# Optimization experiments

Measured on AMD Instinct MI355X. Metric: run time of the kernel, lower is better.

Reference implementation:

```python
import jax, jax.numpy as jnp
import numpy as np

B, F, T, K = 4096, 2048, 16, 8


def setup_inputs() -> dict:
    key = jax.random.key(0)
    k1, k2, k3 = jax.random.split(key, 3)
    h_ens = jax.random.normal(k1, (B, F, T), dtype=jnp.float32)
    # Stacked per-(task, timestep) Linear(num_in_feat, 1) weights and biases.
    # nn.Linear default init ~ U(-1/sqrt(F), 1/sqrt(F)); plain normals are fine for a numeric reference.
    W = jax.random.normal(k2, (K, T, F), dtype=jnp.float32) * (1.0 / np.sqrt(F))
    b = jax.random.normal(k3, (K, T), dtype=jnp.float32) * (1.0 / np.sqrt(F))
    return {"h_ens": h_ens, "W": W, "b": b}


def reference(h_ens, W, b):
    # h_ens: [B, F, T], W: [K, T, F], b: [K, T]
    # logits[b, t, k] = sum_f h_ens[b, f, t] * W[k, t, f] + b[k, t]
    logits = jnp.einsum('bft,ktf->btk', h_ens, W) + b.T[None, :, :]
    return jax.nn.sigmoid(logits)  # [B, T, K]
```

## Files before the change

kernel.cpp:

```cpp
#include <hip/hip_runtime.h>
#include <math.h>

#define B_TOT 4096
#define F_DIM 2048
#define T_DIM 16
#define K_DIM 8
#define NB    4
#define SF    64
#define NSUP  (F_DIM / SF)

__device__ __forceinline__ void gload_lds16(const float* g, float* l) {
    __builtin_amdgcn_global_load_lds(
        (const __attribute__((address_space(1))) void*)g,
        (__attribute__((address_space(3))) void*)l,
        16, 0, 0);
}

__global__ __launch_bounds__(256)
void ta_kernel(const float* __restrict__ h, const float* __restrict__ W,
               const float* __restrict__ bias, float* __restrict__ out)
{
    __shared__ float smem[8192];

    const int tid  = threadIdx.x;
    const int t    = tid & 15;
    const int fres = tid >> 4;
    const int b0   = blockIdx.x * NB;

    float acc[NB][K_DIM];
#pragma unroll
    for (int nb = 0; nb < NB; ++nb)
#pragma unroll
        for (int k = 0; k < K_DIM; ++k) acc[nb][k] = 0.f;

    const int tl = tid >> 4;
    const int j4 = ((tid & 15) - tl) & 15;
    const float* wp = W + tl * F_DIM + j4 * 4;
    float* lp = smem + tid * 4;

    int voff[4];
#pragma unroll
    for (int il = 0; il < 4; ++il)
        voff[il] = t * 64 + ((il * 4 + (fres >> 2) + t) & 15) * 4 + (fres & 3);

    const float* hb = h + (size_t)b0 * (F_DIM * T_DIM) + tid;

    for (int sc = 0; sc < NSUP; ++sc) {
        __syncthreads();
        {
            const float* wpf = wp + sc * SF;
#pragma unroll
            for (int r = 0; r < K_DIM; ++r)
                gload_lds16(wpf + r * (T_DIM * F_DIM), lp + r * 1024);
        }
        __syncthreads();

#pragma unroll
        for (int il = 0; il < 4; ++il) {
            float hv[NB];
#pragma unroll
            for (int nb = 0; nb < NB; ++nb)
                hv[nb] = hb[nb * (F_DIM * T_DIM) + sc * 1024 + il * 256];

            float wv[K_DIM];
#pragma unroll
            for (int k = 0; k < K_DIM; ++k)
                wv[k] = smem[k * 1024 + voff[il]];

#pragma unroll
            for (int nb = 0; nb < NB; ++nb)
#pragma unroll
                for (int k = 0; k < K_DIM; ++k)
                    acc[nb][k] = fmaf(hv[nb], wv[k], acc[nb][k]);
        }
    }

    __syncthreads();
#pragma unroll
    for (int nb = 0; nb < NB; ++nb)
#pragma unroll
        for (int k = 0; k < K_DIM; ++k)
            smem[(nb * 8 + k) * 256 + tid] = acc[nb][k];
    __syncthreads();

#pragma unroll
    for (int rep = 0; rep < 2; ++rep) {
        const int o   = tid + rep * 256;
        const int nb  = o >> 7;
        const int rem = o & 127;
        const int tt  = rem >> 3;
        const int kk  = rem & 7;
        float s = 0.f;
#pragma unroll
        for (int fr = 0; fr < 16; ++fr)
            s += smem[(nb * 8 + kk) * 256 + fr * 16 + tt];
        s += bias[kk * T_DIM + tt];
        s = 1.0f / (1.0f + __expf(-s));
        out[(size_t)(b0 + nb) * (T_DIM * K_DIM) + rem] = s;
    }
}

extern "C" void kernel_launch(void* const* d_in, const int* in_sizes, int n_in,
                              void* d_out, int out_size, void* d_ws, size_t ws_size,
                              hipStream_t stream) {
    const float* h    = (const float*)d_in[0];
    const float* W    = (const float*)d_in[1];
    const float* bias = (const float*)d_in[2];
    float* out = (float*)d_out;
    ta_kernel<<<dim3(B_TOT / NB), dim3(256), 0, stream>>>(h, W, bias, out);
}
```

Before: 691.6 us.

## Double-buffer h loads in registers with float2 per-thread timestep pairs

Each thread now handles two adjacent timesteps, loading h as float2, and prefetches the next super-chunk's h values into a second register buffer while computing the current one. The thread-to-(t,f) mapping changes to 8 timestep pairs by 32 feature lanes, so the final cross-lane reduction sums 32 partials through a reorganized, bank-rotated shared-memory layout done in two passes. The aim is to hide global-load latency of the dominant h stream and widen loads, at the cost of double the accumulator registers (64 plus prefetch buffers), which may reduce occupancy.

```diff
diff --git a/kernel.cpp b/kernel.cpp
--- a/kernel.cpp
+++ b/kernel.cpp
@@ -22,30 +22,47 @@
 {
     __shared__ float smem[8192];
 
-    const int tid  = threadIdx.x;
-    const int t    = tid & 15;
-    const int fres = tid >> 4;
-    const int b0   = blockIdx.x * NB;
+    const int tid = threadIdx.x;
+    const int tp  = tid & 7;
+    const int fr  = tid >> 3;
+    const int b0  = blockIdx.x * NB;
 
-    float acc[NB][K_DIM];
+    float acc[NB][2][K_DIM];
 #pragma unroll
     for (int nb = 0; nb < NB; ++nb)
 #pragma unroll
-        for (int k = 0; k < K_DIM; ++k) acc[nb][k] = 0.f;
+        for (int ts = 0; ts < 2; ++ts)
+#pragma unroll
+            for (int k = 0; k < K_DIM; ++k) acc[nb][ts][k] = 0.f;
 
     const int tl = tid >> 4;
     const int j4 = ((tid & 15) - tl) & 15;
     const float* wp = W + tl * F_DIM + j4 * 4;
     float* lp = smem + tid * 4;
 
-    int voff[4];
+    int voff[2][2];
 #pragma unroll
-    for (int il = 0; il < 4; ++il)
-        voff[il] = t * 64 + ((il * 4 + (fres >> 2) + t) & 15) * 4 + (fres & 3);
+    for (int il = 0; il < 2; ++il)
+#pragma unroll
+        for (int ts = 0; ts < 2; ++ts) {
+            const int t = 2 * tp + ts;
+            voff[il][ts] = t * 64 + ((il * 8 + (fr >> 2) + t) & 15) * 4 + (fr & 3);
+        }
 
-    const float* hb = h + (size_t)b0 * (F_DIM * T_DIM) + tid;
+    const float2* hb = (const float2*)h + (size_t)b0 * 16384 + fr * 8 + tp;
 
-    for (int sc = 0; sc < NSUP; ++sc) {
+    float2 hA[2][NB], hB[2][NB];
+
+    auto loadh = [&](float2 (&buf)[2][NB], int sc) {
+#pragma unroll
+        for (int il = 0; il < 2; ++il)
+#pragma unroll
+            for (int nb = 0; nb < NB; ++nb)
+                buf[il][nb] = hb[(size_t)nb * 16384 + sc * 512 + il * 256];
+    };
+
+    auto tile = [&](int sc, float2 (&cur)[2][NB], float2 (&nxt)[2][NB],
+                    bool pf, int scn) {
         __syncthreads();
         {
             const float* wpf = wp + sc * SF;
@@ -54,49 +71,54 @@
                 gload_lds16(wpf + r * (T_DIM * F_DIM), lp + r * 1024);
         }
         __syncthreads();
+        if (pf) loadh(nxt, scn);
 
 #pragma unroll
-        for (int il = 0; il < 4; ++il) {
-            float hv[NB];
+        for (int il = 0; il < 2; ++il)
 #pragma unroll
-            for (int nb = 0; nb < NB; ++nb)
-                hv[nb] = hb[nb * (F_DIM * T_DIM) + sc * 1024 + il * 256];
+            for (int ts = 0; ts < 2; ++ts) {
+                float wv[K_DIM];
+#pragma unroll
+                for (int k = 0; k < K_DIM; ++k)
+                    wv[k] = smem[k * 1024 + voff[il][ts]];
+#pragma unroll
+                for (int nb = 0; nb < NB; ++nb) {
+                    const float hx = ts ? cur[il][nb].y : cur[il][nb].x;
+#pragma unroll
+                    for (int k = 0; k < K_DIM; ++k)
+                        acc[nb][ts][k] = fmaf(hx, wv[k], acc[nb][ts][k]);
+                }
+            }
+    };
 
-            float wv[K_DIM];
-#pragma unroll
-            for (int k = 0; k < K_DIM; ++k)
-                wv[k] = smem[k * 1024 + voff[il]];
+    loadh(hA, 0);
+    for (int sc = 0; sc < NSUP; sc += 2) {
+        tile(sc,     hA, hB, true,          sc + 1);
+        tile(sc + 1, hB, hA, sc + 2 < NSUP, sc + 2);
+    }
 
 #pragma unroll
-            for (int nb = 0; nb < NB; ++nb)
+    for (int c = 0; c < 2; ++c) {
+        __syncthreads();
+#pragma unroll
+        for (int nbl = 0; nbl < 2; ++nbl)
+#pragma unroll
+            for (int ts = 0; ts < 2; ++ts) {
+                const int t = 2 * tp + ts;
 #pragma unroll
                 for (int k = 0; k < K_DIM; ++k)
-                    acc[nb][k] = fmaf(hv[nb], wv[k], acc[nb][k]);
-        }
-    }
-
-    __syncthreads();
-#pragma unroll
-    for (int nb = 0; nb < NB; ++nb)
-#pragma unroll
-        for (int k = 0; k < K_DIM; ++k)
-            smem[(nb * 8 + k) * 256 + tid] = acc[nb][k];
-    __syncthreads();
-
-#pragma unroll
-    for (int rep = 0; rep < 2; ++rep) {
-        const int o   = tid + rep * 256;
-        const int nb  = o >> 7;
-        const int rem = o & 127;
-        const int tt  = rem >> 3;
-        const int kk  = rem & 7;
+                    smem[(nbl * 16 + t) * 256 + k * 32 + ((fr + tp * 4) & 31)]
+                        = acc[c * 2 + nbl][ts][k];
+            }
+        __syncthreads();
+        const int nbl = tid >> 7, rem = tid & 127, tt = rem >> 3, kk = rem & 7;
         float s = 0.f;
 #pragma unroll
-        for (int fr = 0; fr < 16; ++fr)
-            s += smem[(nb * 8 + kk) * 256 + fr * 16 + tt];
+        for (int j = 0; j < 32; ++j)
+            s += smem[(nbl * 16 + tt) * 256 + kk * 32 + ((tid + j) & 31)];
         s += bias[kk * T_DIM + tt];
         s = 1.0f / (1.0f + __expf(-s));
-        out[(size_t)(b0 + nb) * (T_DIM * K_DIM) + rem] = s;
+        out[(size_t)(b0 + c * 2 + nbl) * (T_DIM * K_DIM) + rem] = s;
     }
 }
 
```

After: 697.0 us. About the same (+0.8%).
